# Kernel tuning notes

Measured on AMD Instinct MI355X. Metric: run time of the kernel, lower is better.

Reference implementation:

```python
import jax, jax.numpy as jnp
import numpy as np


def log_g(x):
    # log of g(x) = relu(x)+0.5 for x>=0, sigmoid(x) for x<0 (continuous minGRU activation)
    return jnp.where(x >= 0, jnp.log(jax.nn.relu(x) + 0.5), -jax.nn.softplus(-x))


def parallel_scan_log(log_coeffs, log_values):
    # log_coeffs: [B,T,H], log_values: [B,T+1,H]
    a_star = jnp.pad(jnp.cumsum(log_coeffs, axis=1), ((0, 0), (1, 0), (0, 0)))  # [B,T+1,H]
    log_h = a_star + jax.lax.cumlogsumexp(log_values - a_star, axis=1)
    return jnp.exp(log_h)  # [B,T+1,H]


def setup_inputs() -> dict:
    key = jax.random.key(0)
    B, T, D, H = 8, 4096, 1024, 1024
    k1, k2, k3, k4, k5, k6 = jax.random.split(key, 6)
    scale = 1.0 / np.sqrt(D)
    return {
        "x": jax.random.normal(k1, (B, T, D), dtype=jnp.float32),
        "h_0": jax.random.uniform(k2, (B, 1, H), dtype=jnp.float32),
        "W_z": jax.random.uniform(k3, (H, D), minval=-scale, maxval=scale, dtype=jnp.float32),
        "b_z": jax.random.uniform(k4, (H,), minval=-scale, maxval=scale, dtype=jnp.float32),
        "W_h": jax.random.uniform(k5, (H, D), minval=-scale, maxval=scale, dtype=jnp.float32),
        "b_h": jax.random.uniform(k6, (H,), minval=-scale, maxval=scale, dtype=jnp.float32),
    }


def reference(x, h_0, W_z, b_z, W_h, b_h):
    # k = linear_z(x)
    k = jnp.einsum('btd,hd->bth', x, W_z) + b_z                 # [B,T,H]
    log_z = -jax.nn.softplus(-k)                                # log sigmoid(k)
    log_coeffs = -jax.nn.softplus(k)                            # log (1 - sigmoid(k))
    log_h_0 = log_g(h_0)                                        # [B,1,H]
    log_tilde_h = log_g(jnp.einsum('btd,hd->bth', x, W_h) + b_h)  # [B,T,H]
    log_values = jnp.concatenate([log_h_0, log_z + log_tilde_h], axis=1)  # [B,T+1,H]
    h = parallel_scan_log(log_coeffs, log_values)               # [B,T+1,H]
    return h
```

## Files before the change

### kernel.cpp

```cpp
#include <hip/hip_runtime.h>
#include <stdint.h>

#define B_ 8
#define T_ 4096
#define D_ 1024
#define H_ 1024
#define M_ (B_*T_)
#define K_ D_
#define N_ H_
#define TC 64
#define NC (T_/TC)

typedef short short8 __attribute__((ext_vector_type(8)));
typedef float f32x4 __attribute__((ext_vector_type(4)));
typedef unsigned short ushort8v __attribute__((ext_vector_type(8)));

__device__ __forceinline__ float bf2f(unsigned short u) {
    union { unsigned int i; float f; } x; x.i = ((unsigned int)u) << 16; return x.f;
}
__device__ __forceinline__ unsigned short f2bf(float f) {
    union { float f; unsigned int i; } x; x.f = f;
    unsigned int u = x.i;
    unsigned int r = u + 0x7fffu + ((u >> 16) & 1u);
    return (unsigned short)(r >> 16);
}
__device__ __forceinline__ void gld_lds16(const unsigned short* g, unsigned short* l) {
    __builtin_amdgcn_global_load_lds(
        (const __attribute__((address_space(1))) void*)(const void*)g,
        (__attribute__((address_space(3))) void*)(void*)l, 16, 0, 0);
}
__device__ __forceinline__ float gfun(float x) {
    return x >= 0.f ? x + 0.5f : 1.f / (1.f + __expf(-x));
}

__global__ void cvt_kernel(const float* __restrict__ src, unsigned short* __restrict__ dst, int n4) {
    int i = blockIdx.x * blockDim.x + threadIdx.x;
    const int stride = gridDim.x * blockDim.x;
    for (; i < n4; i += stride) {
        float4 v = ((const float4*)src)[i];
        ushort4 o;
        o.x = f2bf(v.x); o.y = f2bf(v.y); o.z = f2bf(v.z); o.w = f2bf(v.w);
        ((ushort4*)dst)[i] = o;
    }
}

__global__ __launch_bounds__(256) void gemm_kernel(
    const unsigned short* __restrict__ Xb,
    const unsigned short* __restrict__ Wzb,
    const unsigned short* __restrict__ Whb,
    const float* __restrict__ bz, const float* __restrict__ bh,
    unsigned short* __restrict__ KzOut, unsigned short* __restrict__ KhOut)
{
    __shared__ __align__(16) unsigned short lds_a[128 * 32];
    __shared__ __align__(16) unsigned short lds_b[128 * 32];

    const int bm = blockIdx.x;
    const int bn = blockIdx.y;
    const int mat = blockIdx.z;
    const unsigned short* Wb = mat ? Whb : Wzb;
    const float* bias = mat ? bh : bz;
    unsigned short* Out = mat ? KhOut : KzOut;

    const int tid = threadIdx.x;
    const int w = tid >> 6, lane = tid & 63;
    const int wm = w >> 1, wn = w & 1;

    f32x4 acc[4][4];
#pragma unroll
    for (int i = 0; i < 4; i++)
#pragma unroll
        for (int j = 0; j < 4; j++) acc[i][j] = (f32x4){0.f, 0.f, 0.f, 0.f};

    const int kcs = ((lane & 3) ^ ((lane >> 3) & 3)) * 8;
    const int r0 = (w * 2 + 0) * 16 + (lane >> 2);
    const int r1 = (w * 2 + 1) * 16 + (lane >> 2);
    const unsigned short* gA0 = Xb + (size_t)(bm * 128 + r0) * K_ + kcs;
    const unsigned short* gA1 = Xb + (size_t)(bm * 128 + r1) * K_ + kcs;
    const unsigned short* gB0 = Wb + (size_t)(bn * 128 + r0) * K_ + kcs;
    const unsigned short* gB1 = Wb + (size_t)(bn * 128 + r1) * K_ + kcs;
    unsigned short* la0 = &lds_a[(w * 2 + 0) * 512];
    unsigned short* la1 = &lds_a[(w * 2 + 1) * 512];
    unsigned short* lb0 = &lds_b[(w * 2 + 0) * 512];
    unsigned short* lb1 = &lds_b[(w * 2 + 1) * 512];

    const int sw = ((lane >> 4) ^ ((lane >> 1) & 3)) * 8;
    const unsigned short* ra = &lds_a[(wm * 64 + (lane & 15)) * 32 + sw];
    const unsigned short* rb = &lds_b[(wn * 64 + (lane & 15)) * 32 + sw];

    for (int k0 = 0; k0 < K_; k0 += 32) {
        __syncthreads();
        gld_lds16(gA0 + k0, la0);
        gld_lds16(gA1 + k0, la1);
        gld_lds16(gB0 + k0, lb0);
        gld_lds16(gB1 + k0, lb1);
        __syncthreads();

        short8 af[4], bfr[4];
#pragma unroll
        for (int im = 0; im < 4; im++) af[im] = *(const short8*)(ra + im * 16 * 32);
#pragma unroll
        for (int in = 0; in < 4; in++) bfr[in] = *(const short8*)(rb + in * 16 * 32);
#pragma unroll
        for (int im = 0; im < 4; im++)
#pragma unroll
            for (int in = 0; in < 4; in++)
                acc[im][in] = __builtin_amdgcn_mfma_f32_16x16x32_bf16(af[im], bfr[in], acc[im][in], 0, 0, 0);
    }

#pragma unroll
    for (int in = 0; in < 4; in++) {
        const int n = bn * 128 + wn * 64 + in * 16 + (lane & 15);
        const float bb = bias[n];
#pragma unroll
        for (int im = 0; im < 4; im++) {
            const int mq = bm * 32 + wm * 16 + im * 4 + (lane >> 4);
            ushort4 o;
            o.x = f2bf(acc[im][in][0] + bb);
            o.y = f2bf(acc[im][in][1] + bb);
            o.z = f2bf(acc[im][in][2] + bb);
            o.w = f2bf(acc[im][in][3] + bb);
            *(ushort4*)(Out + ((size_t)mq * N_ + n) * 4) = o;
        }
    }
}


__global__ __launch_bounds__(256) void scanA_kernel(const unsigned short* __restrict__ Kz,
                                                    const unsigned short* __restrict__ Kh,
                                                    float* __restrict__ Fc, float* __restrict__ Vc)
{
    const int c = blockIdx.x, b = blockIdx.y;
    const int hb = threadIdx.x * 4;
    float F[4] = {1.f, 1.f, 1.f, 1.f}, V[4] = {0.f, 0.f, 0.f, 0.f};
    size_t base = ((size_t)(b * 1024 + c * (TC / 4)) * N_ + hb) * 4;
    for (int q = 0; q < TC / 4; q++) {
        ushort8v z0 = *(const ushort8v*)(Kz + base);
        ushort8v z1 = *(const ushort8v*)(Kz + base + 8);
        ushort8v h0v = *(const ushort8v*)(Kh + base);
        ushort8v h1v = *(const ushort8v*)(Kh + base + 8);
        base += (size_t)N_ * 4;
#pragma unroll
        for (int r = 0; r < 4; r++) {
            float kzf[4] = {bf2f(z0[r]), bf2f(z0[4 + r]), bf2f(z1[r]), bf2f(z1[4 + r])};
            float khf[4] = {bf2f(h0v[r]), bf2f(h0v[4 + r]), bf2f(h1v[r]), bf2f(h1v[4 + r])};
#pragma unroll
            for (int j = 0; j < 4; j++) {
                float f = 1.f / (1.f + __expf(kzf[j]));
                float v = (1.f - f) * gfun(khf[j]);
                V[j] = f * V[j] + v;
                F[j] *= f;
            }
        }
    }
    size_t o = ((size_t)(b * NC + c)) * H_ + hb;
    *(float4*)(Fc + o) = make_float4(F[0], F[1], F[2], F[3]);
    *(float4*)(Vc + o) = make_float4(V[0], V[1], V[2], V[3]);
}

__global__ __launch_bounds__(256) void scanB_kernel(const float* __restrict__ h0,
                                                    const float* __restrict__ Fc,
                                                    const float* __restrict__ Vc,
                                                    float* __restrict__ Carry,
                                                    float* __restrict__ Out)
{
    const int b = blockIdx.x;
    const int h = threadIdx.x * 4;
    float cy[4];
#pragma unroll
    for (int j = 0; j < 4; j++) cy[j] = gfun(h0[(size_t)b * H_ + h + j]);
    *(float4*)(Out + (size_t)b * (T_ + 1) * H_ + h) = make_float4(cy[0], cy[1], cy[2], cy[3]);
    for (int c = 0; c < NC; c++) {
        size_t o = ((size_t)(b * NC + c)) * H_ + h;
        *(float4*)(Carry + o) = make_float4(cy[0], cy[1], cy[2], cy[3]);
        float4 F4 = *(const float4*)(Fc + o);
        float4 V4 = *(const float4*)(Vc + o);
        cy[0] = F4.x * cy[0] + V4.x;
        cy[1] = F4.y * cy[1] + V4.y;
        cy[2] = F4.z * cy[2] + V4.z;
        cy[3] = F4.w * cy[3] + V4.w;
    }
}

__global__ __launch_bounds__(256) void scanC_kernel(const unsigned short* __restrict__ Kz,
                                                    const unsigned short* __restrict__ Kh,
                                                    const float* __restrict__ Carry,
                                                    float* __restrict__ Out)
{
    const int c = blockIdx.x, b = blockIdx.y;
    const int hb = threadIdx.x * 4;
    float cy[4];
    {
        float4 c4 = *(const float4*)(Carry + ((size_t)(b * NC + c)) * H_ + hb);
        cy[0] = c4.x; cy[1] = c4.y; cy[2] = c4.z; cy[3] = c4.w;
    }
    size_t base = ((size_t)(b * 1024 + c * (TC / 4)) * N_ + hb) * 4;
    size_t ob = ((size_t)(b * (T_ + 1) + c * TC + 1)) * H_ + hb;
    for (int q = 0; q < TC / 4; q++) {
        ushort8v z0 = *(const ushort8v*)(Kz + base);
        ushort8v z1 = *(const ushort8v*)(Kz + base + 8);
        ushort8v h0v = *(const ushort8v*)(Kh + base);
        ushort8v h1v = *(const ushort8v*)(Kh + base + 8);
        base += (size_t)N_ * 4;
#pragma unroll
        for (int r = 0; r < 4; r++) {
            float kzf[4] = {bf2f(z0[r]), bf2f(z0[4 + r]), bf2f(z1[r]), bf2f(z1[4 + r])};
            float khf[4] = {bf2f(h0v[r]), bf2f(h0v[4 + r]), bf2f(h1v[r]), bf2f(h1v[4 + r])};
#pragma unroll
            for (int j = 0; j < 4; j++) {
                float f = 1.f / (1.f + __expf(kzf[j]));
                float v = (1.f - f) * gfun(khf[j]);
                cy[j] = f * cy[j] + v;
            }
            *(float4*)(Out + ob) = make_float4(cy[0], cy[1], cy[2], cy[3]);
            ob += H_;
        }
    }
}

extern "C" void kernel_launch(void* const* d_in, const int* in_sizes, int n_in,
                              void* d_out, int out_size, void* d_ws, size_t ws_size,
                              hipStream_t stream)
{
    const float* x  = (const float*)d_in[0];
    const float* h0 = (const float*)d_in[1];
    const float* Wz = (const float*)d_in[2];
    const float* bz = (const float*)d_in[3];
    const float* Wh = (const float*)d_in[4];
    const float* bh = (const float*)d_in[5];
    float* out = (float*)d_out;

    char* ws = (char*)d_ws;
    unsigned short* xb  = (unsigned short*)ws; ws += (size_t)M_ * K_ * 2;
    unsigned short* wzb = (unsigned short*)ws; ws += (size_t)N_ * K_ * 2;
    unsigned short* whb = (unsigned short*)ws; ws += (size_t)N_ * K_ * 2;
    unsigned short* kz  = (unsigned short*)ws; ws += (size_t)M_ * N_ * 2;
    unsigned short* kh  = (unsigned short*)ws; ws += (size_t)M_ * N_ * 2;
    float* Fc    = (float*)ws; ws += (size_t)B_ * NC * H_ * 4;
    float* Vc    = (float*)ws; ws += (size_t)B_ * NC * H_ * 4;
    float* Carry = (float*)ws; ws += (size_t)B_ * NC * H_ * 4;

    cvt_kernel<<<2048, 256, 0, stream>>>(x, xb, M_ * K_ / 4);
    cvt_kernel<<<256, 256, 0, stream>>>(Wz, wzb, N_ * K_ / 4);
    cvt_kernel<<<256, 256, 0, stream>>>(Wh, whb, N_ * K_ / 4);

    dim3 gg(M_ / 128, N_ / 128, 2);
    gemm_kernel<<<gg, 256, 0, stream>>>(xb, wzb, whb, bz, bh, kz, kh);

    scanA_kernel<<<dim3(NC, B_), 256, 0, stream>>>(kz, kh, Fc, Vc);
    scanB_kernel<<<B_, 256, 0, stream>>>(h0, Fc, Vc, Carry, out);
    scanC_kernel<<<dim3(NC, B_), 256, 0, stream>>>(kz, kh, Carry, out);
}
```

Baseline: 499.2 us.

## Rewrite GEMM as 256x256 tile, double-buffered LDS pipeline with 8 waves

Replaces the 128x128, single-buffered, sync-per-k-step GEMM with a 256x256 tile, 512 threads and a K-step of 64. LDS is double-buffered, and global-to-LDS loads for the next k-tile are interleaved with MFMA quads using explicit barriers, vmcnt waits and setprio. The aim is to hide global load latency and raise arithmetic intensity per byte moved. In exchange it uses 128KB of LDS and many accumulator registers, and its correctness depends on hand-placed waitcnt counts.

```diff
diff --git a/kernel.cpp b/kernel.cpp
--- a/kernel.cpp
+++ b/kernel.cpp
@@ -10,6 +10,7 @@
 #define N_ H_
 #define TC 64
 #define NC (T_/TC)
+#define NKT (K_/64)
 
 typedef short short8 __attribute__((ext_vector_type(8)));
 typedef float f32x4 __attribute__((ext_vector_type(4)));
@@ -44,15 +45,18 @@
     }
 }
 
-__global__ __launch_bounds__(256) void gemm_kernel(
+#define SB() __builtin_amdgcn_sched_barrier(0)
+#define BAR() do { SB(); __builtin_amdgcn_s_barrier(); SB(); } while (0)
+
+__global__ __launch_bounds__(512, 2) void gemm_kernel(
     const unsigned short* __restrict__ Xb,
     const unsigned short* __restrict__ Wzb,
     const unsigned short* __restrict__ Whb,
     const float* __restrict__ bz, const float* __restrict__ bh,
     unsigned short* __restrict__ KzOut, unsigned short* __restrict__ KhOut)
 {
-    __shared__ __align__(16) unsigned short lds_a[128 * 32];
-    __shared__ __align__(16) unsigned short lds_b[128 * 32];
+    __shared__ __align__(16) unsigned short ldsA[2][256 * 64];
+    __shared__ __align__(16) unsigned short ldsB[2][256 * 64];
 
     const int bm = blockIdx.x;
     const int bn = blockIdx.y;
@@ -63,62 +67,130 @@
 
     const int tid = threadIdx.x;
     const int w = tid >> 6, lane = tid & 63;
-    const int wm = w >> 1, wn = w & 1;
-
-    f32x4 acc[4][4];
-#pragma unroll
-    for (int i = 0; i < 4; i++)
-#pragma unroll
-        for (int j = 0; j < 4; j++) acc[i][j] = (f32x4){0.f, 0.f, 0.f, 0.f};
-
-    const int kcs = ((lane & 3) ^ ((lane >> 3) & 3)) * 8;
-    const int r0 = (w * 2 + 0) * 16 + (lane >> 2);
-    const int r1 = (w * 2 + 1) * 16 + (lane >> 2);
-    const unsigned short* gA0 = Xb + (size_t)(bm * 128 + r0) * K_ + kcs;
-    const unsigned short* gA1 = Xb + (size_t)(bm * 128 + r1) * K_ + kcs;
-    const unsigned short* gB0 = Wb + (size_t)(bn * 128 + r0) * K_ + kcs;
-    const unsigned short* gB1 = Wb + (size_t)(bn * 128 + r1) * K_ + kcs;
-    unsigned short* la0 = &lds_a[(w * 2 + 0) * 512];
-    unsigned short* la1 = &lds_a[(w * 2 + 1) * 512];
-    unsigned short* lb0 = &lds_b[(w * 2 + 0) * 512];
-    unsigned short* lb1 = &lds_b[(w * 2 + 1) * 512];
-
-    const int sw = ((lane >> 4) ^ ((lane >> 1) & 3)) * 8;
-    const unsigned short* ra = &lds_a[(wm * 64 + (lane & 15)) * 32 + sw];
-    const unsigned short* rb = &lds_b[(wn * 64 + (lane & 15)) * 32 + sw];
-
-    for (int k0 = 0; k0 < K_; k0 += 32) {
-        __syncthreads();
-        gld_lds16(gA0 + k0, la0);
-        gld_lds16(gA1 + k0, la1);
-        gld_lds16(gB0 + k0, lb0);
-        gld_lds16(gB1 + k0, lb1);
-        __syncthreads();
-
-        short8 af[4], bfr[4];
-#pragma unroll
-        for (int im = 0; im < 4; im++) af[im] = *(const short8*)(ra + im * 16 * 32);
-#pragma unroll
-        for (int in = 0; in < 4; in++) bfr[in] = *(const short8*)(rb + in * 16 * 32);
-#pragma unroll
-        for (int im = 0; im < 4; im++)
-#pragma unroll
-            for (int in = 0; in < 4; in++)
-                acc[im][in] = __builtin_amdgcn_mfma_f32_16x16x32_bf16(af[im], bfr[in], acc[im][in], 0, 0, 0);
-    }
-
-#pragma unroll
-    for (int in = 0; in < 4; in++) {
-        const int n = bn * 128 + wn * 64 + in * 16 + (lane & 15);
+    const int wm = w >> 2, wn = w & 3;
+
+    const int srow = lane >> 3;
+    const int schunk = ((lane & 7) ^ srow) << 3;
+    const unsigned short* gA = Xb + (size_t)(bm * 256 + srow) * K_ + schunk;
+    const unsigned short* gB = Wb + (size_t)(bn * 256 + srow) * K_ + schunk;
+
+#define STAGE_A(s, kt, h) do { \
+    gld_lds16(gA + (size_t)((h)*128 + 0*64 + w*8) * K_ + (kt)*64, &ldsA[s][((h)*128 + 0*64 + w*8) * 64]); \
+    gld_lds16(gA + (size_t)((h)*128 + 1*64 + w*8) * K_ + (kt)*64, &ldsA[s][((h)*128 + 1*64 + w*8) * 64]); \
+  } while (0)
+#define STAGE_B(s, kt, h) do { \
+    gld_lds16(gB + (size_t)((h)*128 + 0*64 + w*8) * K_ + (kt)*64, &ldsB[s][((h)*128 + 0*64 + w*8) * 64]); \
+    gld_lds16(gB + (size_t)((h)*128 + 1*64 + w*8) * K_ + (kt)*64, &ldsB[s][((h)*128 + 1*64 + w*8) * 64]); \
+  } while (0)
+
+    const int lrow = lane & 15;
+    const int q = lane >> 4;
+    const int sw0 = (q ^ (lane & 7)) << 3;
+
+#define LDA(s, fm, kh) (*(const short8*)&ldsA[s][(wm*128 + (fm)*16 + lrow) * 64 + (sw0 ^ ((kh)*32))])
+#define LDB(s, fn, kh) (*(const short8*)&ldsB[s][(wn*64  + (fn)*16 + lrow) * 64 + (sw0 ^ ((kh)*32))])
+
+#define RD_A4(s, fmb) do { \
+    _Pragma("unroll") for (int f = 0; f < 4; ++f) { Ar[f][0] = LDA(s, (fmb)+f, 0); Ar[f][1] = LDA(s, (fmb)+f, 1); } \
+  } while (0)
+#define RD_B2(s, fnb) do { \
+    _Pragma("unroll") for (int g = 0; g < 2; ++g) { Br[(fnb)+g][0] = LDB(s, (fnb)+g, 0); Br[(fnb)+g][1] = LDB(s, (fnb)+g, 1); } \
+  } while (0)
+
+#define QUAD(mb, nb) do { \
+    __builtin_amdgcn_s_setprio(1); \
+    _Pragma("unroll") for (int f = 0; f < 4; ++f) { \
+      _Pragma("unroll") for (int g = 0; g < 2; ++g) { \
+        acc[(mb)+f][(nb)+g] = __builtin_amdgcn_mfma_f32_16x16x32_bf16(Ar[f][0], Br[(nb)+g][0], acc[(mb)+f][(nb)+g], 0, 0, 0); \
+        acc[(mb)+f][(nb)+g] = __builtin_amdgcn_mfma_f32_16x16x32_bf16(Ar[f][1], Br[(nb)+g][1], acc[(mb)+f][(nb)+g], 0, 0, 0); \
+      } \
+    } \
+    __builtin_amdgcn_s_setprio(0); \
+  } while (0)
+
+    f32x4 acc[8][4];
+#pragma unroll
+    for (int i = 0; i < 8; ++i)
+#pragma unroll
+        for (int j = 0; j < 4; ++j) acc[i][j] = (f32x4){0.f, 0.f, 0.f, 0.f};
+    short8 Ar[4][2], Br[4][2];
+
+    STAGE_B(0, 0, 0); STAGE_B(0, 0, 1);
+    STAGE_A(0, 0, 0); STAGE_A(0, 0, 1);
+    STAGE_B(1, 1, 0); STAGE_B(1, 1, 1);
+    SB();
+    asm volatile("s_waitcnt vmcnt(4)" ::: "memory");
+    BAR();
+
+#pragma unroll 1
+    for (int i = 0; i < 8; ++i) {
+        const int kt1 = 2 * i + 1;
+        const int kt2 = 2 * i + 2;
+        const int kt3 = 2 * i + 3;
+        const bool st = (i < 7);
+
+        RD_A4(0, 0); RD_B2(0, 0);
+        STAGE_A(1, kt1, 0);
+        BAR();
+        QUAD(0, 0);
+        BAR();
+        RD_B2(0, 2);
+        STAGE_A(1, kt1, 1);
+        BAR();
+        QUAD(0, 2);
+        BAR();
+        RD_A4(0, 4);
+        if (st) STAGE_B(0, kt2, 0);
+        BAR();
+        QUAD(4, 0);
+        BAR();
+        if (st) {
+            STAGE_B(0, kt2, 1);
+            SB();
+            asm volatile("s_waitcnt vmcnt(4)" ::: "memory");
+        } else {
+            asm volatile("s_waitcnt vmcnt(0)" ::: "memory");
+        }
+        BAR();
+        QUAD(4, 2);
+        BAR();
+        RD_A4(1, 0); RD_B2(1, 0);
+        if (st) STAGE_A(0, kt2, 0);
+        BAR();
+        QUAD(0, 0);
+        BAR();
+        RD_B2(1, 2);
+        if (st) STAGE_A(0, kt2, 1);
+        BAR();
+        QUAD(0, 2);
+        BAR();
+        RD_A4(1, 4);
+        if (st) STAGE_B(1, kt3, 0);
+        BAR();
+        QUAD(4, 0);
+        BAR();
+        if (st) {
+            STAGE_B(1, kt3, 1);
+            SB();
+            asm volatile("s_waitcnt vmcnt(4)" ::: "memory");
+        }
+        BAR();
+        QUAD(4, 2);
+        BAR();
+    }
+
+#pragma unroll
+    for (int fn = 0; fn < 4; ++fn) {
+        const int n = bn * 256 + wn * 64 + fn * 16 + lrow;
         const float bb = bias[n];
 #pragma unroll
-        for (int im = 0; im < 4; im++) {
-            const int mq = bm * 32 + wm * 16 + im * 4 + (lane >> 4);
+        for (int fm = 0; fm < 8; ++fm) {
+            const int mq = bm * 64 + wm * 32 + fm * 4 + q;
             ushort4 o;
-            o.x = f2bf(acc[im][in][0] + bb);
-            o.y = f2bf(acc[im][in][1] + bb);
-            o.z = f2bf(acc[im][in][2] + bb);
-            o.w = f2bf(acc[im][in][3] + bb);
+            o.x = f2bf(acc[fm][fn][0] + bb);
+            o.y = f2bf(acc[fm][fn][1] + bb);
+            o.z = f2bf(acc[fm][fn][2] + bb);
+            o.w = f2bf(acc[fm][fn][3] + bb);
             *(ushort4*)(Out + ((size_t)mq * N_ + n) * 4) = o;
         }
     }
@@ -243,8 +315,8 @@
     cvt_kernel<<<256, 256, 0, stream>>>(Wz, wzb, N_ * K_ / 4);
     cvt_kernel<<<256, 256, 0, stream>>>(Wh, whb, N_ * K_ / 4);
 
-    dim3 gg(M_ / 128, N_ / 128, 2);
-    gemm_kernel<<<gg, 256, 0, stream>>>(xb, wzb, whb, bz, bh, kz, kh);
+    dim3 gg(M_ / 256, N_ / 256, 2);
+    gemm_kernel<<<gg, 512, 0, stream>>>(xb, wzb, whb, bz, bh, kz, kh);
 
     scanA_kernel<<<dim3(NC, B_), 256, 0, stream>>>(kz, kh, Fc, Vc);
     scanB_kernel<<<B_, 256, 0, stream>>>(h0, Fc, Vc, Carry, out);
```

After: 466.9 us. 1.07x faster.
